# Optimization experiments

Measured on AMD Instinct MI355X. Metric: run time of the kernel, lower is better.

Reference implementation:

```python
import jax, jax.numpy as jnp
import numpy as np

N, E, IN, OUT, EF = 20000, 100000, 32, 32, 16
NEG = -1e30  # finite sentinel for masked scores (avoids inf*0 grads)


def setup_inputs() -> dict:
    key = jax.random.key(0)
    ks = jax.random.split(key, 8)
    return {
        "feat": jax.random.normal(ks[0], (N, IN), jnp.float32),
        "efeat": jax.random.normal(ks[1], (E, EF), jnp.float32),
        "src": jax.random.randint(ks[2], (E,), 0, N, dtype=jnp.int32),
        "dst": jax.random.randint(ks[3], (E,), 0, N, dtype=jnp.int32),
        "etype": jax.random.randint(ks[4], (E,), 0, 2, dtype=jnp.int32),
        "attn_w": jax.random.normal(ks[5], (2 * IN, 1), jnp.float32) * 0.1,
        "attn_b": jnp.zeros((1,), jnp.float32),
        "ef1_w": jax.random.normal(ks[6], (EF, IN * OUT), jnp.float32) * 0.05,
        "ef1_b": jnp.zeros((IN * OUT,), jnp.float32),
        "ef2_w": jax.random.normal(ks[7], (EF, IN * OUT), jnp.float32) * 0.05,
        "ef2_b": jnp.zeros((IN * OUT,), jnp.float32),
        "bias": jnp.zeros((OUT,), jnp.float32),
    }


def reference(feat, efeat, src, dst, etype, attn_w, attn_b,
              ef1_w, ef1_b, ef2_w, ef2_b, bias):
    n_nodes = feat.shape[0]
    z_src = feat[src]                      # [E, IN] gather src features
    z_dst = feat[dst]                      # [E, IN] gather dst features
    # per-edge scalar attention score: leaky_relu(Linear(cat(z_src, z_dst)))
    score = jax.nn.leaky_relu(
        (jnp.concatenate([z_src, z_dst], axis=1) @ attn_w + attn_b)[:, 0]
    )  # [E]

    def relation_agg(mask, w, b):
        # edge-specific weight matrices: [E, IN, OUT]
        We = (efeat @ w + b).reshape(E, IN, OUT)
        # message per edge = src_feat @ W_e  (sum over IN commutes with attn)
        msg = jnp.einsum('ei,eio->eo', z_src, We)        # [E, OUT]
        # segment softmax over incoming edges of this relation per dst node
        s = jnp.where(mask, score, NEG)
        smax = jax.ops.segment_max(s, dst, num_segments=n_nodes)
        ex = jnp.where(mask, jnp.exp(s - smax[dst]), 0.0)
        den = jax.ops.segment_sum(ex, dst, num_segments=n_nodes)
        alpha = ex / jnp.where(den > 0, den, 1.0)[dst]   # [E]
        # attention-weighted scatter-sum to dst nodes
        return jax.ops.segment_sum(alpha[:, None] * msg, dst,
                                   num_segments=n_nodes)  # [N, OUT]

    rst = relation_agg(etype == 0, ef1_w, ef1_b) \
        + relation_agg(etype == 1, ef2_w, ef2_b) \
        + bias
    return rst
```

## Files before the change

kernel.cpp:

```cpp
#include <hip/hip_runtime.h>

typedef __attribute__((ext_vector_type(8))) short bf16x8;
typedef __attribute__((ext_vector_type(16))) float f32x16;
typedef __attribute__((ext_vector_type(2))) float f32x2;

__device__ __forceinline__ unsigned short f2b(float x) {
    unsigned u = __float_as_uint(x);
    unsigned r = (u + 0x7fffu + ((u >> 16) & 1u)) >> 16;
    return (unsigned short)r;
}
__device__ __forceinline__ unsigned f2b2(float lo, float hi) {
    return (unsigned)f2b(lo) | ((unsigned)f2b(hi) << 16);
}
__device__ __forceinline__ float b2f(unsigned short u) {
    return __uint_as_float((unsigned)u << 16);
}
__device__ __forceinline__ f32x2 pk_fma(f32x2 a, f32x2 b, f32x2 c) {
    f32x2 d;
    asm("v_pk_fma_f32 %0, %1, %2, %3" : "=v"(d) : "v"(a), "v"(b), "v"(c));
    return d;
}

__global__ void k_zero(int* __restrict__ hist, int* __restrict__ lkb,
                       const float* __restrict__ feat, const float* __restrict__ attn_w,
                       const float* __restrict__ w1, const float* __restrict__ b1,
                       const float* __restrict__ w2, const float* __restrict__ b2,
                       float* __restrict__ ps, float* __restrict__ pd,
                       unsigned short* __restrict__ PA, int N) {
    int idx = blockIdx.x * blockDim.x + threadIdx.x;
    int n2q = (2 * N + 3) >> 2;
    if (idx < n2q) ((int4*)hist)[idx] = make_int4(0, 0, 0, 0);
    if (idx < 16) ((int4*)lkb)[idx] = make_int4(0, 0, 0, 0);
    if (idx < N) {
        const float4* zp = (const float4*)(feat + (long)idx * 32);
        const float4* aw = (const float4*)attn_w;
        float a = 0.f, b = 0.f;
        #pragma unroll
        for (int j = 0; j < 8; ++j) {
            float4 z = zp[j], wa = aw[j], wb = aw[8 + j];
            a = fmaf(z.x, wa.x, a); a = fmaf(z.y, wa.y, a);
            a = fmaf(z.z, wa.z, a); a = fmaf(z.w, wa.w, a);
            b = fmaf(z.x, wb.x, b); b = fmaf(z.y, wb.y, b);
            b = fmaf(z.z, wb.z, b); b = fmaf(z.w, wb.w, b);
        }
        ps[idx] = a; pd[idx] = b;
    }
    if (idx < 2 * 17 * 2 * 64) {
        int l = idx & 63;
        int x = idx >> 6;
        int h = x & 1; x >>= 1;
        int t = x % 17;
        int r = x / 17;
        const float* W = r ? w2 : w1;
        const float* B = r ? b2 : b1;
        int o = l & 31;
        int kb = h * 16 + (l >> 5) * 8;
        unsigned short v[8];
        #pragma unroll
        for (int j = 0; j < 8; ++j) {
            int i = kb + j;
            float sv = (t < 16) ? W[t * 1024 + i * 32 + o] : B[i * 32 + o];
            v[j] = f2b(sv);
        }
        uint4 pack;
        pack.x = (unsigned)v[0] | ((unsigned)v[1] << 16);
        pack.y = (unsigned)v[2] | ((unsigned)v[3] << 16);
        pack.z = (unsigned)v[4] | ((unsigned)v[5] << 16);
        pack.w = (unsigned)v[6] | ((unsigned)v[7] << 16);
        *((uint4*)PA + idx) = pack;
    }
}

__global__ void k_hist(const int* __restrict__ dst, const int* __restrict__ etype,
                       int* __restrict__ hist, int E, int N) {
    int e = blockIdx.x * blockDim.x + threadIdx.x;
    if (e < E) atomicAdd(&hist[etype[e] * N + dst[e]], 1);
}

__global__ __launch_bounds__(256) void k_scan(const int* __restrict__ hist,
                                              int* __restrict__ rowptr,
                                              int* __restrict__ cursor,
                                              int* __restrict__ lkb, int n, int E) {
    __shared__ int s[256];
    __shared__ int soff;
    int t = threadIdx.x, b = blockIdx.x;
    int i0 = b * 1024 + t * 4;
    int4 hv = make_int4(0, 0, 0, 0);
    if (i0 + 3 < n) hv = *(const int4*)(hist + i0);
    else {
        if (i0 + 0 < n) hv.x = hist[i0 + 0];
        if (i0 + 1 < n) hv.y = hist[i0 + 1];
        if (i0 + 2 < n) hv.z = hist[i0 + 2];
        if (i0 + 3 < n) hv.w = hist[i0 + 3];
    }
    int tot = hv.x + hv.y + hv.z + hv.w;
    s[t] = tot;
    __syncthreads();
    for (int d = 1; d < 256; d <<= 1) {
        int x = (t >= d) ? s[t - d] : 0;
        __syncthreads();
        s[t] += x;
        __syncthreads();
    }
    if (t == 255) atomicExch(&lkb[b], s[255] + 1);
    if (t < 64) {
        int v = 0;
        if (t < b) {
            int p;
            do { p = atomicAdd(&lkb[t], 0); } while (p == 0);
            v = p - 1;
        }
        #pragma unroll
        for (int d = 32; d >= 1; d >>= 1) v += __shfl_down(v, d);
        if (t == 0) soff = v;
    }
    __syncthreads();
    int run = s[t] - tot + soff;
    if (i0 + 0 < n) { rowptr[i0 + 0] = run; cursor[i0 + 0] = run; } run += hv.x;
    if (i0 + 1 < n) { rowptr[i0 + 1] = run; cursor[i0 + 1] = run; } run += hv.y;
    if (i0 + 2 < n) { rowptr[i0 + 2] = run; cursor[i0 + 2] = run; } run += hv.z;
    if (i0 + 3 < n) { rowptr[i0 + 3] = run; cursor[i0 + 3] = run; }
    if (t == 0 && b == 0) rowptr[n] = E;
}

__global__ void k_score(const int* __restrict__ src, const int* __restrict__ dst,
                        const int* __restrict__ etype,
                        const float* __restrict__ ps, const float* __restrict__ pd,
                        const float* __restrict__ attn_b,
                        int* __restrict__ cursor, int* __restrict__ sortidx,
                        float* __restrict__ exs, int E, int N) {
    int e = blockIdx.x * blockDim.x + threadIdx.x;
    if (e >= E) return;
    int d = dst[e];
    float sc = ps[src[e]] + pd[d] + attn_b[0];
    sc = sc >= 0.f ? sc : 0.01f * sc;
    float v = __expf(sc);
    int key = etype[e] * N + d;
    int pos = atomicAdd(&cursor[key], 1);
    sortidx[pos] = e;
    exs[pos] = v;
}

__global__ __launch_bounds__(256) void k_msg(
    const float* __restrict__ feat, const float* __restrict__ efeat,
    const int* __restrict__ src, const unsigned short* __restrict__ PA,
    const int* __restrict__ sortidx, const int* __restrict__ rowptr,
    unsigned short* __restrict__ wmsg, int E, int N) {
    int r = blockIdx.y;
    int cnt0 = rowptr[N];
    int relstart = r ? cnt0 : 0;
    int count = r ? (E - cnt0) : cnt0;
    int base = blockIdx.x * 128;
    if (count <= 0 || base >= count) return;

    int tid = threadIdx.x;
    int lane = tid & 63;
    int ecol = (tid >> 6) * 32 + (lane & 31);
    int kb = (lane >> 5) * 8;
    int gi = base + ecol;
    bool valid = gi < count;
    int e = sortidx[relstart + min(gi, count - 1)];
    int sn = src[e];

    const float4* zp = (const float4*)(feat + (long)sn * 32);
    float4 z0 = zp[kb >> 2], z1 = zp[(kb >> 2) + 1];
    float4 z2 = zp[(kb >> 2) + 4], z3 = zp[(kb >> 2) + 5];
    uint4 pb0, pb1;
    pb0.x = f2b2(z0.x, z0.y); pb0.y = f2b2(z0.z, z0.w);
    pb0.z = f2b2(z1.x, z1.y); pb0.w = f2b2(z1.z, z1.w);
    pb1.x = f2b2(z2.x, z2.y); pb1.y = f2b2(z2.z, z2.w);
    pb1.z = f2b2(z3.x, z3.y); pb1.w = f2b2(z3.z, z3.w);
    bf16x8 b0 = *(bf16x8*)&pb0, b1 = *(bf16x8*)&pb1;

    const float4* up = (const float4*)(efeat + (long)e * 16);
    float4 u0 = up[0], u1 = up[1], u2 = up[2], u3 = up[3];
    float uu[16] = { u0.x, u0.y, u0.z, u0.w, u1.x, u1.y, u1.z, u1.w,
                     u2.x, u2.y, u2.z, u2.w, u3.x, u3.y, u3.z, u3.w };

    const bf16x8* pa = (const bf16x8*)PA + (long)r * 34 * 64 + lane;

    f32x2 m2[8];
    {
        bf16x8 a0 = pa[32 * 64];
        bf16x8 a1 = pa[33 * 64];
        f32x16 c;
        #pragma unroll
        for (int k = 0; k < 16; ++k) c[k] = 0.f;
        c = __builtin_amdgcn_mfma_f32_32x32x16_bf16(a0, b0, c, 0, 0, 0);
        c = __builtin_amdgcn_mfma_f32_32x32x16_bf16(a1, b1, c, 0, 0, 0);
        #pragma unroll
        for (int k = 0; k < 8; ++k) { m2[k][0] = c[2 * k]; m2[k][1] = c[2 * k + 1]; }
    }
    #pragma unroll 4
    for (int t = 0; t < 16; ++t) {
        bf16x8 a0 = pa[(t * 2 + 0) * 64];
        bf16x8 a1 = pa[(t * 2 + 1) * 64];
        f32x16 c;
        #pragma unroll
        for (int k = 0; k < 16; ++k) c[k] = 0.f;
        c = __builtin_amdgcn_mfma_f32_32x32x16_bf16(a0, b0, c, 0, 0, 0);
        c = __builtin_amdgcn_mfma_f32_32x32x16_bf16(a1, b1, c, 0, 0, 0);
        f32x2 ud; ud[0] = uu[t]; ud[1] = uu[t];
        #pragma unroll
        for (int k = 0; k < 8; ++k) {
            f32x2 cc; cc[0] = c[2 * k]; cc[1] = c[2 * k + 1];
            m2[k] = pk_fma(ud, cc, m2[k]);
        }
    }

    if (valid) {
        unsigned short* wr = wmsg + (long)(relstart + gi) * 32 + kb / 2;
        *(uint2*)(wr +  0) = make_uint2(f2b2(m2[0][0], m2[0][1]), f2b2(m2[1][0], m2[1][1]));
        *(uint2*)(wr +  8) = make_uint2(f2b2(m2[2][0], m2[2][1]), f2b2(m2[3][0], m2[3][1]));
        *(uint2*)(wr + 16) = make_uint2(f2b2(m2[4][0], m2[4][1]), f2b2(m2[5][0], m2[5][1]));
        *(uint2*)(wr + 24) = make_uint2(f2b2(m2[6][0], m2[6][1]), f2b2(m2[7][0], m2[7][1]));
    }
}

__global__ void k_reduce(const int* __restrict__ rowptr, const float* __restrict__ exs,
                         const unsigned short* __restrict__ wmsg,
                         const float* __restrict__ bias,
                         float* __restrict__ out, int N) {
    int tid = blockIdx.x * blockDim.x + threadIdx.x;
    if (tid >= N * 8) return;
    int n = tid >> 3, og = tid & 7;
    float4 acc = ((const float4*)bias)[og];
    #pragma unroll 1
    for (int r = 0; r < 2; ++r) {
        int k = r * N + n;
        int s = rowptr[k], e2 = rowptr[k + 1];
        if (s >= e2) continue;
        float den = 0.f;
        #pragma unroll 1
        for (int p = s; p < e2; ++p) den += exs[p];
        float inv = 1.f / den;
        #pragma unroll 1
        for (int p = s; p < e2; ++p) {
            float w = exs[p] * inv;
            ushort4 m = *(const ushort4*)(wmsg + (long)p * 32 + og * 4);
            acc.x = fmaf(w, b2f(m.x), acc.x);
            acc.y = fmaf(w, b2f(m.y), acc.y);
            acc.z = fmaf(w, b2f(m.z), acc.z);
            acc.w = fmaf(w, b2f(m.w), acc.w);
        }
    }
    ((float4*)out)[tid] = acc;
}

extern "C" void kernel_launch(void* const* d_in, const int* in_sizes, int n_in,
                              void* d_out, int out_size, void* d_ws, size_t ws_size,
                              hipStream_t stream) {
    const float* feat   = (const float*)d_in[0];
    const float* efeat  = (const float*)d_in[1];
    const int*   src    = (const int*)d_in[2];
    const int*   dst    = (const int*)d_in[3];
    const int*   etype  = (const int*)d_in[4];
    const float* attn_w = (const float*)d_in[5];
    const float* attn_b = (const float*)d_in[6];
    const float* ef1_w  = (const float*)d_in[7];
    const float* ef1_b  = (const float*)d_in[8];
    const float* ef2_w  = (const float*)d_in[9];
    const float* ef2_b  = (const float*)d_in[10];
    const float* bias   = (const float*)d_in[11];

    int E = in_sizes[2];
    int N = in_sizes[0] / 32;
    int n2 = 2 * N;
    int nb = (n2 + 1023) / 1024;

    float*          ps      = (float*)d_ws;
    float*          pd      = ps + N;
    unsigned short* PA      = (unsigned short*)(pd + N);
    int*            hist    = (int*)(PA + 2 * 17 * 2 * 64 * 8);
    int*            rowptr  = hist + n2;
    int*            cursor  = rowptr + n2 + 1;
    int*            lkb     = cursor + n2;
    int*            sortidx = lkb + 64;
    float*          exs     = (float*)(sortidx + E);
    unsigned short* wmsg    = (unsigned short*)(((size_t)(exs + E) + 15) & ~(size_t)15);
    float*          out     = (float*)d_out;

    k_zero<<<(N + 255) / 256, 256, 0, stream>>>(hist, lkb, feat, attn_w,
                                                ef1_w, ef1_b, ef2_w, ef2_b,
                                                ps, pd, PA, N);
    k_hist<<<(E + 255) / 256, 256, 0, stream>>>(dst, etype, hist, E, N);
    k_scan<<<nb, 256, 0, stream>>>(hist, rowptr, cursor, lkb, n2, E);
    k_score<<<(E + 255) / 256, 256, 0, stream>>>(src, dst, etype, ps, pd, attn_b,
                                                 cursor, sortidx, exs, E, N);
    dim3 mgrid((E + 127) / 128, 2);
    k_msg<<<mgrid, 256, 0, stream>>>(feat, efeat, src, PA, sortidx, rowptr,
                                     wmsg, E, N);
    k_reduce<<<(N * 8 + 255) / 256, 256, 0, stream>>>(rowptr, exs, wmsg, bias, out, N);
}
```

Measured before the change: 50.23 us.

## Fuse scan with scatter via grid barrier and flatten message grid

Score computation moves into the histogram kernel, which stores a per-edge key and exp value. The scan and scatter kernels are merged into one persistent 128-block kernel that uses a spin-wait grid barrier between the two phases. The message kernel switches from a 2D grid, where half the blocks exit early, to a 1D grid sized to the real per-relation counts. This removes one launch and the idle blocks, but adds extra global traffic for the key and exp buffers and relies on all 128 blocks being co-resident for the barrier.

Measured after the change: 64.96 us. +29.3%, slower.

```diff
diff --git a/kernel.cpp b/kernel.cpp
--- a/kernel.cpp
+++ b/kernel.cpp
@@ -30,7 +30,7 @@
     int idx = blockIdx.x * blockDim.x + threadIdx.x;
     int n2q = (2 * N + 3) >> 2;
     if (idx < n2q) ((int4*)hist)[idx] = make_int4(0, 0, 0, 0);
-    if (idx < 16) ((int4*)lkb)[idx] = make_int4(0, 0, 0, 0);
+    if (idx < 17) ((int4*)lkb)[idx] = make_int4(0, 0, 0, 0);
     if (idx < N) {
         const float4* zp = (const float4*)(feat + (long)idx * 32);
         const float4* aw = (const float4*)attn_w;
@@ -71,74 +71,87 @@
     }
 }
 
-__global__ void k_hist(const int* __restrict__ dst, const int* __restrict__ etype,
-                       int* __restrict__ hist, int E, int N) {
+__global__ void k_hist2(const int* __restrict__ src, const int* __restrict__ dst,
+                        const int* __restrict__ etype,
+                        const float* __restrict__ ps, const float* __restrict__ pd,
+                        const float* __restrict__ attn_b,
+                        int* __restrict__ hist, int* __restrict__ key,
+                        float* __restrict__ exu, int E, int N) {
     int e = blockIdx.x * blockDim.x + threadIdx.x;
-    if (e < E) atomicAdd(&hist[etype[e] * N + dst[e]], 1);
-}
-
-__global__ __launch_bounds__(256) void k_scan(const int* __restrict__ hist,
-                                              int* __restrict__ rowptr,
-                                              int* __restrict__ cursor,
-                                              int* __restrict__ lkb, int n, int E) {
+    if (e >= E) return;
+    int d = dst[e];
+    int k = etype[e] * N + d;
+    float sc = ps[src[e]] + pd[d] + attn_b[0];
+    sc = sc >= 0.f ? sc : 0.01f * sc;
+    key[e] = k;
+    exu[e] = __expf(sc);
+    atomicAdd(&hist[k], 1);
+}
+
+__global__ __launch_bounds__(256) void k_scansc(
+    const int* __restrict__ hist, const int* __restrict__ key,
+    const float* __restrict__ exu,
+    int* __restrict__ rowptr, int* __restrict__ cursor,
+    int* __restrict__ lkb, int* __restrict__ done2,
+    int* __restrict__ sortidx, float* __restrict__ exs,
+    int n, int E, int nb) {
     __shared__ int s[256];
     __shared__ int soff;
     int t = threadIdx.x, b = blockIdx.x;
-    int i0 = b * 1024 + t * 4;
-    int4 hv = make_int4(0, 0, 0, 0);
-    if (i0 + 3 < n) hv = *(const int4*)(hist + i0);
-    else {
-        if (i0 + 0 < n) hv.x = hist[i0 + 0];
-        if (i0 + 1 < n) hv.y = hist[i0 + 1];
-        if (i0 + 2 < n) hv.z = hist[i0 + 2];
-        if (i0 + 3 < n) hv.w = hist[i0 + 3];
-    }
-    int tot = hv.x + hv.y + hv.z + hv.w;
-    s[t] = tot;
+    if (b < nb) {
+        int i0 = b * 1024 + t * 4;
+        int4 hv = make_int4(0, 0, 0, 0);
+        if (i0 + 3 < n) hv = *(const int4*)(hist + i0);
+        else {
+            if (i0 + 0 < n) hv.x = hist[i0 + 0];
+            if (i0 + 1 < n) hv.y = hist[i0 + 1];
+            if (i0 + 2 < n) hv.z = hist[i0 + 2];
+            if (i0 + 3 < n) hv.w = hist[i0 + 3];
+        }
+        int tot = hv.x + hv.y + hv.z + hv.w;
+        s[t] = tot;
+        __syncthreads();
+        for (int d = 1; d < 256; d <<= 1) {
+            int x = (t >= d) ? s[t - d] : 0;
+            __syncthreads();
+            s[t] += x;
+            __syncthreads();
+        }
+        if (t == 255) atomicExch(&lkb[b], s[255] + 1);
+        if (t < 64) {
+            int v = 0;
+            if (t < b) {
+                int p;
+                do { p = atomicAdd(&lkb[t], 0); } while (p == 0);
+                v = p - 1;
+            }
+            #pragma unroll
+            for (int d = 32; d >= 1; d >>= 1) v += __shfl_down(v, d);
+            if (t == 0) soff = v;
+        }
+        __syncthreads();
+        int run = s[t] - tot + soff;
+        if (i0 + 0 < n) { rowptr[i0 + 0] = run; atomicExch(&cursor[i0 + 0], run); } run += hv.x;
+        if (i0 + 1 < n) { rowptr[i0 + 1] = run; atomicExch(&cursor[i0 + 1], run); } run += hv.y;
+        if (i0 + 2 < n) { rowptr[i0 + 2] = run; atomicExch(&cursor[i0 + 2], run); } run += hv.z;
+        if (i0 + 3 < n) { rowptr[i0 + 3] = run; atomicExch(&cursor[i0 + 3], run); }
+        if (t == 0 && b == 0) rowptr[n] = E;
+        __syncthreads();
+        __threadfence();
+        if (t == 0) atomicAdd(done2, 1);
+    }
+    if (t == 0) {
+        while (atomicAdd(done2, 0) < nb) { }
+    }
     __syncthreads();
-    for (int d = 1; d < 256; d <<= 1) {
-        int x = (t >= d) ? s[t - d] : 0;
-        __syncthreads();
-        s[t] += x;
-        __syncthreads();
-    }
-    if (t == 255) atomicExch(&lkb[b], s[255] + 1);
-    if (t < 64) {
-        int v = 0;
-        if (t < b) {
-            int p;
-            do { p = atomicAdd(&lkb[t], 0); } while (p == 0);
-            v = p - 1;
-        }
-        #pragma unroll
-        for (int d = 32; d >= 1; d >>= 1) v += __shfl_down(v, d);
-        if (t == 0) soff = v;
-    }
-    __syncthreads();
-    int run = s[t] - tot + soff;
-    if (i0 + 0 < n) { rowptr[i0 + 0] = run; cursor[i0 + 0] = run; } run += hv.x;
-    if (i0 + 1 < n) { rowptr[i0 + 1] = run; cursor[i0 + 1] = run; } run += hv.y;
-    if (i0 + 2 < n) { rowptr[i0 + 2] = run; cursor[i0 + 2] = run; } run += hv.z;
-    if (i0 + 3 < n) { rowptr[i0 + 3] = run; cursor[i0 + 3] = run; }
-    if (t == 0 && b == 0) rowptr[n] = E;
-}
-
-__global__ void k_score(const int* __restrict__ src, const int* __restrict__ dst,
-                        const int* __restrict__ etype,
-                        const float* __restrict__ ps, const float* __restrict__ pd,
-                        const float* __restrict__ attn_b,
-                        int* __restrict__ cursor, int* __restrict__ sortidx,
-                        float* __restrict__ exs, int E, int N) {
-    int e = blockIdx.x * blockDim.x + threadIdx.x;
-    if (e >= E) return;
-    int d = dst[e];
-    float sc = ps[src[e]] + pd[d] + attn_b[0];
-    sc = sc >= 0.f ? sc : 0.01f * sc;
-    float v = __expf(sc);
-    int key = etype[e] * N + d;
-    int pos = atomicAdd(&cursor[key], 1);
-    sortidx[pos] = e;
-    exs[pos] = v;
+    __threadfence();
+    int stride = gridDim.x * 256;
+    for (int e = b * 256 + t; e < E; e += stride) {
+        int k = key[e];
+        int pos = atomicAdd(&cursor[k], 1);
+        sortidx[pos] = e;
+        exs[pos] = exu[e];
+    }
 }
 
 __global__ __launch_bounds__(256) void k_msg(
@@ -146,12 +159,16 @@
     const int* __restrict__ src, const unsigned short* __restrict__ PA,
     const int* __restrict__ sortidx, const int* __restrict__ rowptr,
     unsigned short* __restrict__ wmsg, int E, int N) {
-    int r = blockIdx.y;
     int cnt0 = rowptr[N];
-    int relstart = r ? cnt0 : 0;
-    int count = r ? (E - cnt0) : cnt0;
-    int base = blockIdx.x * 128;
-    if (count <= 0 || base >= count) return;
+    int cnt1 = E - cnt0;
+    int nb0 = (cnt0 + 127) >> 7;
+    int bi = blockIdx.x;
+    int r, base, count, relstart;
+    if (bi < nb0) { r = 0; base = bi * 128; count = cnt0; relstart = 0; }
+    else {
+        r = 1; base = (bi - nb0) * 128; count = cnt1; relstart = cnt0;
+        if (base >= count) return;
+    }
 
     int tid = threadIdx.x;
     int lane = tid & 63;
@@ -275,7 +292,10 @@
     int*            rowptr  = hist + n2;
     int*            cursor  = rowptr + n2 + 1;
     int*            lkb     = cursor + n2;
-    int*            sortidx = lkb + 64;
+    int*            done2   = lkb + 64;
+    int*            keyb    = lkb + 68;
+    float*          exu     = (float*)(keyb + E);
+    int*            sortidx = (int*)(exu + E);
     float*          exs     = (float*)(sortidx + E);
     unsigned short* wmsg    = (unsigned short*)(((size_t)(exs + E) + 15) & ~(size_t)15);
     float*          out     = (float*)d_out;
@@ -283,12 +303,11 @@
     k_zero<<<(N + 255) / 256, 256, 0, stream>>>(hist, lkb, feat, attn_w,
                                                 ef1_w, ef1_b, ef2_w, ef2_b,
                                                 ps, pd, PA, N);
-    k_hist<<<(E + 255) / 256, 256, 0, stream>>>(dst, etype, hist, E, N);
-    k_scan<<<nb, 256, 0, stream>>>(hist, rowptr, cursor, lkb, n2, E);
-    k_score<<<(E + 255) / 256, 256, 0, stream>>>(src, dst, etype, ps, pd, attn_b,
-                                                 cursor, sortidx, exs, E, N);
-    dim3 mgrid((E + 127) / 128, 2);
-    k_msg<<<mgrid, 256, 0, stream>>>(feat, efeat, src, PA, sortidx, rowptr,
-                                     wmsg, E, N);
+    k_hist2<<<(E + 255) / 256, 256, 0, stream>>>(src, dst, etype, ps, pd, attn_b,
+                                                 hist, keyb, exu, E, N);
+    k_scansc<<<128, 256, 0, stream>>>(hist, keyb, exu, rowptr, cursor, lkb, done2,
+                                      sortidx, exs, n2, E, nb);
+    k_msg<<<(E + 127) / 128 + 2, 256, 0, stream>>>(feat, efeat, src, PA, sortidx,
+                                                   rowptr, wmsg, E, N);
     k_reduce<<<(N * 8 + 255) / 256, 256, 0, stream>>>(rowptr, exs, wmsg, bias, out, N);
 }
```
